# Kernel tuning notes

Measured on AMD Instinct MI355X. Metric: run time of the kernel, lower is better.

The kernel has to match this reference:

```python
import jax, jax.numpy as jnp
import numpy as np

D_MODEL = 1024
N_HEADS = 16
HEAD_DIM = D_MODEL // N_HEADS
MAX_REL = 1024
BATCH = 4
SEQ = 1024


def setup_inputs() -> dict:
    key = jax.random.key(0)
    ks = jax.random.split(key, 12)
    f32 = jnp.float32
    scale = 0.02
    inp = {
        "query": jax.random.normal(ks[0], (BATCH, SEQ, D_MODEL), f32),
        "key": jax.random.normal(ks[1], (BATCH, SEQ, D_MODEL), f32),
        "value": jax.random.normal(ks[2], (BATCH, SEQ, D_MODEL), f32),
        # causal mask: 1 indicates positions to mask (strict upper triangle)
        "attention_mask": jnp.triu(jnp.ones((SEQ, SEQ), jnp.int32), k=1)[None, None],
        "Wq": jax.random.normal(ks[3], (D_MODEL, D_MODEL), f32) * scale,
        "bq": jnp.zeros((D_MODEL,), f32),
        "Wk": jax.random.normal(ks[4], (D_MODEL, D_MODEL), f32) * scale,
        "bk": jnp.zeros((D_MODEL,), f32),
        "Wv": jax.random.normal(ks[5], (D_MODEL, D_MODEL), f32) * scale,
        "bv": jnp.zeros((D_MODEL,), f32),
        "rel_tab": jax.random.normal(ks[6], (MAX_REL, D_MODEL), f32) * scale,
        "Wo": jax.random.normal(ks[7], (D_MODEL, D_MODEL), f32) * scale,
        "bo": jnp.zeros((D_MODEL,), f32),
    }
    return inp


def _relative_positions(rel_tab, seq_len):
    # Mirrors get_relative_positions with max_len = MAX_REL (static ints).
    pad_n = max(seq_len - MAX_REL, 0)
    start = max(MAX_REL - seq_len, 0)
    tail = rel_tab[start:MAX_REL]  # (min(seq_len, MAX_REL), D)
    if pad_n > 0:
        head = jnp.tile(rel_tab[0:1], (pad_n, 1))
        return jnp.concatenate([head, tail], axis=0)
    return tail  # (seq_len, D)


def _skew(pos_raw):
    # pos_raw: (B, H, S, S). Music-Transformer skew trick:
    # pad one column on the left, reshape, drop first row, reshape back.
    B, H, Sq, Sk = pos_raw.shape
    padded = jnp.pad(pos_raw, ((0, 0), (0, 0), (0, 0), (1, 0)))  # (B,H,Sq,Sk+1)
    t = padded.reshape(-1, Sk + 1, Sq)
    return t[:, 1:].reshape(B, H, Sq, Sk)


def reference(query, key, value, attention_mask, Wq, bq, Wk, bk, Wv, bv, rel_tab, Wo, bo):
    B, Sq, D = query.shape
    Sk = key.shape[-2]
    H, hd = N_HEADS, HEAD_DIM

    q = query @ Wq + bq
    k = key @ Wk + bk
    v = value @ Wv + bv
    rel = _relative_positions(rel_tab, Sk)  # (Sk, D)

    # split heads -> (B, H, S, hd); rel -> (H, Sk, hd)
    qh = q.reshape(B, Sq, H, hd).transpose(0, 2, 1, 3)
    kh = k.reshape(B, Sk, H, hd).transpose(0, 2, 1, 3)
    vh = v.reshape(B, Sk, H, hd).transpose(0, 2, 1, 3)
    rh = rel.reshape(Sk, H, hd).transpose(1, 0, 2)

    content = jnp.einsum('bhqd,bhkd->bhqk', qh, kh)
    pos_raw = jnp.einsum('bhqd,hkd->bhqk', qh, rh)
    pos = _skew(pos_raw)

    scale = 1.0 / np.sqrt(hd).astype(np.float32)
    scores = (content + pos) * scale
    scores = jnp.where(attention_mask == 1, jnp.float32(-1e9), scores)
    weights = jax.nn.softmax(scores, axis=-1)

    out = jnp.einsum('bhqk,bhkd->bhqd', weights, vh)
    out = out.transpose(0, 2, 1, 3).reshape(B, Sq, D)
    return out @ Wo + bo
```

## Files before the change

### kernel.cpp

```cpp
#include <hip/hip_runtime.h>
#include <cstddef>
#include <cstdint>


typedef __attribute__((ext_vector_type(8))) short bf16x8;
typedef __attribute__((ext_vector_type(4))) float f32x4;
typedef __attribute__((ext_vector_type(4))) unsigned int u32x4;

using u16 = unsigned short;
using u32 = unsigned int;

#define QSCALE (0.125f * 1.44269504089f)

__device__ __forceinline__ f32x4 mfma16(bf16x8 a, bf16x8 b, f32x4 c) {
  return __builtin_amdgcn_mfma_f32_16x16x32_bf16(a, b, c, 0, 0, 0);
}
__device__ __forceinline__ u32 fbits(float f) {
  union { float f; u32 u; } v; v.f = f; return v.u;
}
__device__ __forceinline__ u16 f2b(float f) { return (u16)((fbits(f) + 0x8000u) >> 16); }
__device__ __forceinline__ u32 pack2(float a, float b) {
  return ((fbits(a) + 0x8000u) >> 16) | ((fbits(b) + 0x8000u) & 0xffff0000u);
}
__device__ __forceinline__ float b2f(u16 u) {
  union { u32 i; float f; } v; v.i = ((u32)u) << 16; return v.f;
}
__device__ __forceinline__ float exp2_fast(float x) {
  float r; asm("v_exp_f32 %0, %1" : "=v"(r) : "v"(x)); return r;
}
__device__ __forceinline__ void gload16(const void* g, void* l) {
  __builtin_amdgcn_global_load_lds(
      (const __attribute__((address_space(1))) u32*)g,
      (__attribute__((address_space(3))) u32*)l, 16, 0, 0);
}

__global__ __launch_bounds__(256) void cvt_qkv(
    const float* __restrict__ a0, const float* __restrict__ a1,
    const float* __restrict__ a2, u16* __restrict__ o0,
    u16* __restrict__ o1, u16* __restrict__ o2) {
  int z = blockIdx.y;
  const float* src = (z == 0) ? a0 : (z == 1) ? a1 : a2;
  u16* dst = (z == 0) ? o0 : (z == 1) ? o1 : o2;
  size_t i = ((size_t)blockIdx.x * 256 + threadIdx.x) * 4;
  f32x4 v = *(const f32x4*)(src + i);
  uint2 pk; pk.x = pack2(v[0], v[1]); pk.y = pack2(v[2], v[3]);
  *(uint2*)(dst + i) = pk;
}

__global__ __launch_bounds__(256) void prep(
    const float* __restrict__ Wq, const float* __restrict__ Wk,
    const float* __restrict__ Wv, const float* __restrict__ rel,
    u16* __restrict__ WqT, u16* __restrict__ WkT, u16* __restrict__ WvT,
    u16* __restrict__ relb) {
  __shared__ __align__(16) u16 tile[64][65];
  int z = blockIdx.z;
  if (z == 3) {
    int blk = blockIdx.y * 16 + blockIdx.x;
    size_t base = (size_t)blk * 4096;
#pragma unroll
    for (int e = 0; e < 4; e++) {
      size_t idx = base + e * 1024 + threadIdx.x * 4;
      f32x4 v = *(const f32x4*)(rel + idx);
      uint2 pk; pk.x = pack2(v[0], v[1]); pk.y = pack2(v[2], v[3]);
      *(uint2*)(relb + idx) = pk;
    }
    return;
  }
  const float* W = (z == 0) ? Wq : (z == 1) ? Wk : Wv;
  u16* T = (z == 0) ? WqT : (z == 1) ? WkT : WvT;
  float sc = (z == 0) ? QSCALE : 1.0f;
  int k0 = blockIdx.x * 64, n0 = blockIdx.y * 64;
  for (int e = threadIdx.x; e < 4096; e += 256) {
    int r = e >> 6, c = e & 63;
    tile[r][c] = f2b(sc * W[(size_t)(k0 + r) * 1024 + n0 + c]);
  }
  __syncthreads();
  for (int e = threadIdx.x; e < 4096; e += 256) {
    int r = e >> 6, c = e & 63;
    T[(size_t)(n0 + r) * 1024 + k0 + c] = tile[c][r];
  }
}

__global__ __launch_bounds__(256) void transpose_wo(
    const float* __restrict__ W, u16* __restrict__ T) {
  __shared__ __align__(16) u16 tile[64][65];
  int k0 = blockIdx.x * 64, n0 = blockIdx.y * 64;
  for (int e = threadIdx.x; e < 4096; e += 256) {
    int r = e >> 6, c = e & 63;
    tile[r][c] = f2b(W[(size_t)(k0 + r) * 1024 + n0 + c]);
  }
  __syncthreads();
  for (int e = threadIdx.x; e < 4096; e += 256) {
    int r = e >> 6, c = e & 63;
    T[(size_t)(n0 + r) * 1024 + k0 + c] = tile[c][r];
  }
}

__device__ __forceinline__ void gemm_epilogue(
    f32x4 (&acc)[4][4], const float* __restrict__ bias, float bscale,
    void* __restrict__ Cv, int layout, int m0, int n0, int wr, int wc,
    int quad, int ln) {
#pragma unroll
  for (int ct = 0; ct < 4; ct++) {
    int n = n0 + wc + 16 * ct + ln;
    float bs = bscale * bias[n];
#pragma unroll
    for (int rt = 0; rt < 4; rt++) {
#pragma unroll
      for (int r = 0; r < 4; r++) {
        int m = m0 + wr + 16 * rt + quad * 4 + r;
        float v = acc[rt][ct][r] + bs;
        if (layout == 0) {
          ((float*)Cv)[(size_t)m * 1024 + n] = v;
        } else {
          int b_ = m >> 10, s = m & 1023, h = n >> 6, d = n & 63;
          size_t idx = (layout == 1)
              ? ((size_t)(b_ * 16 + h) * 1024 + s) * 64 + d
              : ((size_t)(b_ * 16 + h) * 64 + d) * 1024 + s;
          ((u16*)Cv)[idx] = f2b(v);
        }
      }
    }
  }
}

__device__ __forceinline__ void gemm_glds_body(
    const u16* __restrict__ A, const u16* __restrict__ Bt,
    const float* __restrict__ bias, float bscale, void* __restrict__ Cv,
    int layout) {
  __shared__ __align__(16) u16 As[128 * 64];
  __shared__ __align__(16) u16 Bs[128 * 64];
  int m0 = blockIdx.x * 128, n0 = blockIdx.y * 128;
  int tid = threadIdx.x;
  int w = tid >> 6, lane = tid & 63, quad = lane >> 4, ln = lane & 15;
  int wr = (w >> 1) * 64, wc = (w & 1) * 64;

  int rowin = lane >> 3;
  int swz = ((lane & 7) ^ rowin) * 8;

  f32x4 acc[4][4];
#pragma unroll
  for (int i = 0; i < 4; i++)
#pragma unroll
    for (int j = 0; j < 4; j++) { acc[i][j][0]=0.f; acc[i][j][1]=0.f; acc[i][j][2]=0.f; acc[i][j][3]=0.f; }

  const u16* aA = A  + (size_t)(m0 + 32 * w + rowin) * 1024 + swz;
  const u16* aB = Bt + (size_t)(n0 + 32 * w + rowin) * 1024 + swz;

  for (int k0 = 0; k0 < 1024; k0 += 64) {
#pragma unroll
    for (int j = 0; j < 4; j++) {
      gload16(aA + k0 + (size_t)(8 * j) * 1024, &As[(32 * w + 8 * j) * 64]);
      gload16(aB + k0 + (size_t)(8 * j) * 1024, &Bs[(32 * w + 8 * j) * 64]);
    }
    __syncthreads();
#pragma unroll
    for (int kk = 0; kk < 64; kk += 32) {
      int sA = (((quad + (kk >> 3)) ^ (ln & 7))) * 8;
      bf16x8 af[4], bfr[4];
#pragma unroll
      for (int rt = 0; rt < 4; rt++)
        af[rt] = *(const bf16x8*)&As[(wr + 16 * rt + ln) * 64 + sA];
#pragma unroll
      for (int ct = 0; ct < 4; ct++)
        bfr[ct] = *(const bf16x8*)&Bs[(wc + 16 * ct + ln) * 64 + sA];
#pragma unroll
      for (int rt = 0; rt < 4; rt++)
#pragma unroll
        for (int ct = 0; ct < 4; ct++)
          acc[rt][ct] = mfma16(af[rt], bfr[ct], acc[rt][ct]);
    }
    __syncthreads();
  }

  gemm_epilogue(acc, bias, bscale, Cv, layout, m0, n0, wr, wc, quad, ln);
}

__device__ __forceinline__ void gemm128_body_f32(
    const float* __restrict__ Av, const u16* __restrict__ Bt,
    const float* __restrict__ bias, float bscale, void* __restrict__ Cv,
    int layout) {
  __shared__ __align__(16) u16 As[128][72];
  __shared__ __align__(16) u16 Bs[128][72];
  int m0 = blockIdx.x * 128, n0 = blockIdx.y * 128;
  int tid = threadIdx.x;
  int w = tid >> 6, lane = tid & 63, quad = lane >> 4, ln = lane & 15;
  int wr = (w >> 1) * 64, wc = (w & 1) * 64;
  int sr = tid >> 1, seg = (tid & 1) * 32;

  f32x4 acc[4][4];
#pragma unroll
  for (int i = 0; i < 4; i++)
#pragma unroll
    for (int j = 0; j < 4; j++) { acc[i][j][0]=0.f; acc[i][j][1]=0.f; acc[i][j][2]=0.f; acc[i][j][3]=0.f; }

  for (int k0 = 0; k0 < 1024; k0 += 64) {
    {
      const float* ap = Av + (size_t)(m0 + sr) * 1024 + k0 + seg;
      u32 pk[16];
#pragma unroll
      for (int j = 0; j < 8; j++) {
        f32x4 v = *(const f32x4*)(ap + 4 * j);
        pk[2 * j]     = pack2(v[0], v[1]);
        pk[2 * j + 1] = pack2(v[2], v[3]);
      }
      u32* d = (u32*)&As[sr][seg];
#pragma unroll
      for (int j = 0; j < 4; j++) *(u32x4*)(d + 4 * j) = *(u32x4*)(pk + 4 * j);
    }
    {
      const u16* bp = Bt + (size_t)(n0 + sr) * 1024 + k0 + seg;
#pragma unroll
      for (int j = 0; j < 4; j++)
        *(bf16x8*)&Bs[sr][seg + 8 * j] = *(const bf16x8*)(bp + 8 * j);
    }
    __syncthreads();
#pragma unroll
    for (int kk = 0; kk < 64; kk += 32) {
      bf16x8 af[4], bfr[4];
#pragma unroll
      for (int rt = 0; rt < 4; rt++)
        af[rt] = *(const bf16x8*)&As[wr + 16 * rt + ln][kk + quad * 8];
#pragma unroll
      for (int ct = 0; ct < 4; ct++)
        bfr[ct] = *(const bf16x8*)&Bs[wc + 16 * ct + ln][kk + quad * 8];
#pragma unroll
      for (int rt = 0; rt < 4; rt++)
#pragma unroll
        for (int ct = 0; ct < 4; ct++)
          acc[rt][ct] = mfma16(af[rt], bfr[ct], acc[rt][ct]);
    }
    __syncthreads();
  }

  gemm_epilogue(acc, bias, bscale, Cv, layout, m0, n0, wr, wc, quad, ln);
}

__global__ __launch_bounds__(256) void gemm_qkv_f32(
    const float* q, const float* k, const float* v, const u16* WT,
    const float* bq, const float* bk, const float* bv,
    u16* Qp, u16* Kp, u16* Vt) {
  int z = blockIdx.z;
  const float* A = (z == 0) ? q : (z == 1) ? k : v;
  const u16* Bt = WT + (size_t)z * (1024 * 1024);
  const float* bias = (z == 0) ? bq : (z == 1) ? bk : bv;
  float bscale = (z == 0) ? QSCALE : 1.0f;
  void* C = (z == 0) ? (void*)Qp : (z == 1) ? (void*)Kp : (void*)Vt;
  gemm128_body_f32(A, Bt, bias, bscale, C, (z == 2) ? 2 : 1);
}

__global__ __launch_bounds__(256) void gemm_qkv_bf(
    const u16* qb, const u16* kb, const u16* vb, const u16* WT,
    const float* bq, const float* bk, const float* bv,
    u16* Qp, u16* Kp, u16* Vt) {
  int z = blockIdx.z;
  const u16* A = (z == 0) ? qb : (z == 1) ? kb : vb;
  const u16* Bt = WT + (size_t)z * (1024 * 1024);
  const float* bias = (z == 0) ? bq : (z == 1) ? bk : bv;
  float bscale = (z == 0) ? QSCALE : 1.0f;
  void* C = (z == 0) ? (void*)Qp : (z == 1) ? (void*)Kp : (void*)Vt;
  gemm_glds_body(A, Bt, bias, bscale, C, (z == 2) ? 2 : 1);
}

__global__ __launch_bounds__(256) void gemm_out(
    const u16* A, const u16* Bt, const float* bias, float* C) {
  gemm_glds_body(A, Bt, bias, 1.0f, C, 0);
}

#define BSTRIDE 332
#define PSTRIDE 280

__global__ __launch_bounds__(256) void attn_v2(
    const u16* __restrict__ Q, const u16* __restrict__ K,
    const u16* __restrict__ Vt, const u16* __restrict__ RB,
    u16* __restrict__ att) {
  __shared__ __align__(16) u16 lPR[64 * BSTRIDE];
  __shared__ __align__(16) u16 lP[64 * PSTRIDE];

  int bh = blockIdx.x;
  int qt = 15 - blockIdx.y;
  int b = bh >> 4, h = bh & 15;
  int tid = threadIdx.x;
  int w = tid >> 6, lane = tid & 63, quad = lane >> 4, ln = lane & 15;

  const u16* Qb = Q + (size_t)bh * 65536;
  const u16* Kb = K + (size_t)bh * 65536;
  const u16* Vb = Vt + (size_t)bh * 65536;
  const u16* Rb = RB + h * 64;

  int row0 = 16 * w + quad * 4;
  int i0 = qt * 64;
  int R0f = 960 - i0;

  int qrow = i0 + 16 * w + ln;
  bf16x8 qa0 = *(const bf16x8*)(Qb + (size_t)qrow * 64 + quad * 8);
  bf16x8 qa1 = *(const bf16x8*)(Qb + (size_t)qrow * 64 + 32 + quad * 8);

  bf16x8 ones;
#pragma unroll
  for (int i = 0; i < 8; i++) ones[i] = (short)0x3F80;

  f32x4 o[4], lacc;
#pragma unroll
  for (int c = 0; c < 4; c++) { o[c][0]=0.f; o[c][1]=0.f; o[c][2]=0.f; o[c][3]=0.f; }
  lacc[0]=0.f; lacc[1]=0.f; lacc[2]=0.f; lacc[3]=0.f;

#pragma unroll 1
  for (int js = 0; js <= i0; js += 256) {
    int ntiles = ((i0 - js) >> 6) + 1;
    if (ntiles > 4) ntiles = 4;
    int base = R0f + js;

    int G = 4 * (ntiles + 1);
#pragma unroll 1
    for (int g = 0; g < G; g++) {
      int rrow = base + 16 * g + ln;
      int rl = rrow > 1023 ? 1023 : rrow;
      const u16* Rrow = Rb + (size_t)rl * 1024 + quad * 8;
      f32x4 a; a[0]=0.f; a[1]=0.f; a[2]=0.f; a[3]=0.f;
      a = mfma16(qa0, *(const bf16x8*)(Rrow), a);
      a = mfma16(qa1, *(const bf16x8*)(Rrow + 32), a);
#pragma unroll
      for (int r = 0; r < 4; r++)
        lPR[(row0 + r) * BSTRIDE + 16 * g + ln] = f2b(a[r]);
    }
    asm volatile("s_waitcnt lgkmcnt(0)" ::: "memory");

#pragma unroll
    for (int t = 0; t < 4; t++) {
      if (t < ntiles) {
        int j0 = js + 64 * t;
        bf16x8 kf[4][2];
#pragma unroll
        for (int c = 0; c < 4; c++) {
          const u16* Krow = Kb + (size_t)(j0 + 16 * c + ln) * 64 + quad * 8;
          kf[c][0] = *(const bf16x8*)(Krow);
          kf[c][1] = *(const bf16x8*)(Krow + 32);
        }
        f32x4 sc[4];
#pragma unroll
        for (int c = 0; c < 4; c++) {
          f32x4 a; a[0]=0.f; a[1]=0.f; a[2]=0.f; a[3]=0.f;
          a = mfma16(qa0, kf[c][0], a);
          a = mfma16(qa1, kf[c][1], a);
          sc[c] = a;
        }
        bool diag = (j0 == i0);
        int cbs = 64 * t + 63;
#pragma unroll
        for (int r = 0; r < 4; r++) {
          int ii = row0 + r;
#pragma unroll
          for (int c = 0; c < 4; c++) {
            int jj = 16 * c + ln;
            float s = sc[c][r] + b2f(lPR[ii * BSTRIDE + cbs - ii + jj]);
            float p = (diag && jj > ii) ? 0.f : exp2_fast(s);
            lP[ii * PSTRIDE + 64 * t + 16 * c + ln] = f2b(p);
          }
        }
      }
    }
    asm volatile("s_waitcnt lgkmcnt(0)" ::: "memory");

    int KC = 2 * ntiles;
#pragma unroll 1
    for (int kc = 0; kc < KC; kc++) {
      bf16x8 pa = *(const bf16x8*)&lP[(16 * w + ln) * PSTRIDE + 32 * kc + quad * 8];
      lacc = mfma16(pa, ones, lacc);
#pragma unroll
      for (int c = 0; c < 4; c++) {
        const u16* Vrow = Vb + (size_t)(16 * c + ln) * 1024 + js + 32 * kc + quad * 8;
        o[c] = mfma16(pa, *(const bf16x8*)(Vrow), o[c]);
      }
    }
    asm volatile("s_waitcnt lgkmcnt(0)" ::: "memory");
  }

#pragma unroll
  for (int c = 0; c < 4; c++) {
#pragma unroll
    for (int r = 0; r < 4; r++) {
      int i_abs = i0 + row0 + r;
      att[((size_t)(b * 1024 + i_abs)) * 1024 + h * 64 + 16 * c + ln] =
          f2b(o[c][r] / lacc[r]);
    }
  }
}

extern "C" void kernel_launch(void* const* d_in, const int* in_sizes, int n_in,
                              void* d_out, int out_size, void* d_ws, size_t ws_size,
                              hipStream_t stream) {
  const float* query = (const float*)d_in[0];
  const float* key   = (const float*)d_in[1];
  const float* value = (const float*)d_in[2];
  const float* Wq = (const float*)d_in[4];
  const float* bq = (const float*)d_in[5];
  const float* Wk = (const float*)d_in[6];
  const float* bk = (const float*)d_in[7];
  const float* Wv = (const float*)d_in[8];
  const float* bv = (const float*)d_in[9];
  const float* RT = (const float*)d_in[10];
  const float* Wo = (const float*)d_in[11];
  const float* bo = (const float*)d_in[12];
  float* out = (float*)d_out;

  const size_t EM = 1024 * 1024;
  u16* ws   = (u16*)d_ws;
  u16* WT   = ws;
  u16* relb = ws + 3 * EM;
  u16* Kp   = ws + 4 * EM;
  u16* Vtp  = ws + 8 * EM;
  u16* Qp   = (u16*)d_out;
  u16* WoT  = ws;

  prep<<<dim3(16, 16, 4), 256, 0, stream>>>(Wq, Wk, Wv, RT,
                                            WT, WT + EM, WT + 2 * EM, relb);

  if (ws_size >= (size_t)48 * 1024 * 1024) {
    u16* qb = ws + 12 * EM;
    u16* kb = ws + 16 * EM;
    u16* vb = ws + 20 * EM;
    cvt_qkv<<<dim3(4096, 3), 256, 0, stream>>>(query, key, value, qb, kb, vb);
    gemm_qkv_bf<<<dim3(32, 8, 3), 256, 0, stream>>>(qb, kb, vb, WT,
                                                    bq, bk, bv, Qp, Kp, Vtp);
    u16* attw = ws + 12 * EM;
    attn_v2<<<dim3(64, 16), 256, 0, stream>>>(Qp, Kp, Vtp, relb, attw);
    transpose_wo<<<dim3(16, 16), 256, 0, stream>>>(Wo, WoT);
    gemm_out<<<dim3(32, 8), 256, 0, stream>>>(attw, WoT, bo, out);
  } else {
    gemm_qkv_f32<<<dim3(32, 8, 3), 256, 0, stream>>>(query, key, value, WT,
                                                     bq, bk, bv, Qp, Kp, Vtp);
    u16* attb = (u16*)d_out + 4 * EM;
    u16* attc = ws + 4 * EM;
    attn_v2<<<dim3(64, 16), 256, 0, stream>>>(Qp, Kp, Vtp, relb, attb);
    hipMemcpyAsync(attc, attb, 8 * 1024 * 1024, hipMemcpyDeviceToDevice, stream);
    transpose_wo<<<dim3(16, 16), 256, 0, stream>>>(Wo, WoT);
    gemm_out<<<dim3(32, 8), 256, 0, stream>>>(attc, WoT, bo, out);
  }
}
```

Before: 300.7 us.

## Keep skewed relative-position scores in registers via ds_bpermute instead of LDS

Removes the LDS staging buffer for relative-position scores. Each wave now computes only the rel-pos tiles it needs, realigns them with cross-lane ds_bpermute rotations plus a select against the previous tile, and keeps the skewed biases packed as bf16 in registers. It also adds a launch-bounds occupancy hint of 4 blocks. This cuts LDS traffic and LDS footprint, allowing more blocks per CU, at the cost of many more VGPRs for the fully unrolled 16-entry register array and the risk of spilling.

```diff
diff --git a/kernel.cpp b/kernel.cpp
--- a/kernel.cpp
+++ b/kernel.cpp
@@ -17,6 +17,9 @@
 }
 __device__ __forceinline__ u32 fbits(float f) {
   union { float f; u32 u; } v; v.f = f; return v.u;
+}
+__device__ __forceinline__ float uif(u32 u) {
+  union { u32 u; float f; } v; v.u = u; return v.f;
 }
 __device__ __forceinline__ u16 f2b(float f) { return (u16)((fbits(f) + 0x8000u) >> 16); }
 __device__ __forceinline__ u32 pack2(float a, float b) {
@@ -267,14 +270,12 @@
   gemm_glds_body(A, Bt, bias, 1.0f, C, 0);
 }
 
-#define BSTRIDE 332
 #define PSTRIDE 280
 
-__global__ __launch_bounds__(256) void attn_v2(
+__global__ __launch_bounds__(256, 4) void attn_v2(
     const u16* __restrict__ Q, const u16* __restrict__ K,
     const u16* __restrict__ Vt, const u16* __restrict__ RB,
     u16* __restrict__ att) {
-  __shared__ __align__(16) u16 lPR[64 * BSTRIDE];
   __shared__ __align__(16) u16 lP[64 * PSTRIDE];
 
   int bh = blockIdx.x;
@@ -292,6 +293,15 @@
   int i0 = qt * 64;
   int R0f = 960 - i0;
 
+  int vaddr[4];
+  bool cond[4];
+#pragma unroll
+  for (int r = 0; r < 4; r++) {
+    int Kq = 15 - 4 * quad - r;
+    vaddr[r] = (((lane & 48) | ((Kq + ln) & 15))) << 2;
+    cond[r] = (Kq + ln) >= 16;
+  }
+
   int qrow = i0 + 16 * w + ln;
   bf16x8 qa0 = *(const bf16x8*)(Qb + (size_t)qrow * 64 + quad * 8);
   bf16x8 qa1 = *(const bf16x8*)(Qb + (size_t)qrow * 64 + 32 + quad * 8);
@@ -309,22 +319,38 @@
   for (int js = 0; js <= i0; js += 256) {
     int ntiles = ((i0 - js) >> 6) + 1;
     if (ntiles > 4) ntiles = 4;
-    int base = R0f + js;
-
-    int G = 4 * (ntiles + 1);
-#pragma unroll 1
-    for (int g = 0; g < G; g++) {
-      int rrow = base + 16 * g + ln;
-      int rl = rrow > 1023 ? 1023 : rrow;
-      const u16* Rrow = Rb + (size_t)rl * 1024 + quad * 8;
-      f32x4 a; a[0]=0.f; a[1]=0.f; a[2]=0.f; a[3]=0.f;
-      a = mfma16(qa0, *(const bf16x8*)(Rrow), a);
-      a = mfma16(qa1, *(const bf16x8*)(Rrow + 32), a);
-#pragma unroll
-      for (int r = 0; r < 4; r++)
-        lPR[(row0 + r) * BSTRIDE + 16 * g + ln] = f2b(a[r]);
-    }
-    asm volatile("s_waitcnt lgkmcnt(0)" ::: "memory");
+    int borig = R0f + js + 48 - 16 * w;
+    int mtop = 4 * ntiles;
+
+    u32 Bp[16][2];
+    f32x4 prev;
+    prev[0]=0.f; prev[1]=0.f; prev[2]=0.f; prev[3]=0.f;
+#pragma unroll
+    for (int m = 0; m <= 16; m++) {
+      if (m <= mtop) {
+        int rrow = borig + 16 * m + ln;
+        int rl = rrow > 1023 ? 1023 : rrow;
+        const u16* Rrow = Rb + (size_t)rl * 1024 + quad * 8;
+        f32x4 a; a[0]=0.f; a[1]=0.f; a[2]=0.f; a[3]=0.f;
+        a = mfma16(qa0, *(const bf16x8*)(Rrow), a);
+        a = mfma16(qa1, *(const bf16x8*)(Rrow + 32), a);
+        f32x4 rot;
+#pragma unroll
+        for (int r = 0; r < 4; r++) {
+          int rv = __builtin_amdgcn_ds_bpermute(vaddr[r], (int)fbits(a[r]));
+          rot[r] = uif((u32)rv);
+        }
+        if (m >= 1) {
+          float b0 = cond[0] ? rot[0] : prev[0];
+          float b1 = cond[1] ? rot[1] : prev[1];
+          float b2 = cond[2] ? rot[2] : prev[2];
+          float b3 = cond[3] ? rot[3] : prev[3];
+          Bp[m - 1][0] = pack2(b0, b1);
+          Bp[m - 1][1] = pack2(b2, b3);
+        }
+        prev = rot;
+      }
+    }
 
 #pragma unroll
     for (int t = 0; t < 4; t++) {
@@ -346,16 +372,19 @@
           sc[c] = a;
         }
         bool diag = (j0 == i0);
-        int cbs = 64 * t + 63;
-#pragma unroll
-        for (int r = 0; r < 4; r++) {
-          int ii = row0 + r;
-#pragma unroll
-          for (int c = 0; c < 4; c++) {
-            int jj = 16 * c + ln;
-            float s = sc[c][r] + b2f(lPR[ii * BSTRIDE + cbs - ii + jj]);
+#pragma unroll
+        for (int c = 0; c < 4; c++) {
+          u32 pk0 = Bp[4 * t + c][0];
+          u32 pk1 = Bp[4 * t + c][1];
+          int jj = 16 * c + ln;
+#pragma unroll
+          for (int r = 0; r < 4; r++) {
+            u16 bv = (u16)((r == 0) ? pk0 : (r == 1) ? (pk0 >> 16)
+                           : (r == 2) ? pk1 : (pk1 >> 16));
+            float s = sc[c][r] + b2f(bv);
+            int ii = row0 + r;
             float p = (diag && jj > ii) ? 0.f : exp2_fast(s);
-            lP[ii * PSTRIDE + 64 * t + 16 * c + ln] = f2b(p);
+            lP[ii * PSTRIDE + 64 * t + jj] = f2b(p);
           }
         }
       }
```

After: 310.0 us. +3.1%, slower.
